# Performance work log

Hardware: AMD Instinct MI355X
Metric: run time of the kernel (lower is better)

Reference implementation:

```python
import jax, jax.numpy as jnp
import numpy as np

B, C, H, W = 1, 256, 96, 96
C8 = C // 8
N = H * W


def setup_inputs() -> dict:
    key = jax.random.key(0)
    ks = jax.random.split(key, 12)
    inp = {
        "x": jax.random.normal(ks[0], (B, C, H, W), jnp.float32),
        "x_encoder": jax.random.normal(ks[1], (B, C, H, W), jnp.float32),
        # 1x1 conv params (weight stored as [out, in] matrices)
        "q_w": jax.random.normal(ks[2], (C8, C), jnp.float32) * 0.05,
        "q_b": jax.random.normal(ks[3], (C8,), jnp.float32) * 0.05,
        "k_w": jax.random.normal(ks[4], (C8, C), jnp.float32) * 0.05,
        "k_b": jax.random.normal(ks[5], (C8,), jnp.float32) * 0.05,
        "v_w": jax.random.normal(ks[6], (C, C), jnp.float32) * 0.05,
        "v_b": jax.random.normal(ks[7], (C,), jnp.float32) * 0.05,
        # positional bias parameters
        "h_pos": jax.random.normal(ks[8], (1, C8, H, 1), jnp.float32),
        "w_pos": jax.random.normal(ks[9], (1, C8, 1, W), jnp.float32),
        # gamma is zero-init in the module; use a random scalar for a non-trivial test
        "gamma": jax.random.normal(ks[10], (1,), jnp.float32),
    }
    return inp


def reference(x, x_encoder, q_w, q_b, k_w, k_b, v_w, v_b, h_pos, w_pos, gamma):
    b, c, h, w = x.shape
    n = h * w
    c8 = q_w.shape[0]
    # 1x1 convs == per-pixel linear maps
    query = (jnp.einsum('bchw,oc->bohw', x, q_w) + q_b[None, :, None, None])
    query = query.reshape(b, c8, n).transpose(0, 2, 1)            # [B, N, C8]
    key = (jnp.einsum('bchw,oc->bohw', x_encoder, k_w) + k_b[None, :, None, None])
    key = key.reshape(b, c8, n)                                   # [B, C8, N]
    # positional bias: broadcast-add then flatten, same as (height+width).view
    pos = (h_pos + w_pos).reshape(1, c8, n)                       # [1, C8, N]
    # energy = Q K^T + Q pos  ==  Q (K + pos)
    energy = jnp.einsum('bnc,bcm->bnm', query, key + pos)         # [B, N, N]
    attention = jax.nn.softmax(energy, axis=-1)
    value = (jnp.einsum('bchw,oc->bohw', x_encoder, v_w) + v_b[None, :, None, None])
    value = value.reshape(b, c, n)                                # [B, C, N]
    out = jnp.einsum('bcm,bnm->bcn', value, attention)            # [B, C, N]
    out = out.reshape(b, c, w, h)  # matches torch .view(B, C, W, H)
    return gamma * out + x
```

## Files before the change

### kernel.cpp

```cpp
#include <hip/hip_runtime.h>
#include <hip/hip_bf16.h>

#define NN 9216
#define CC 256
#define LOG2E 1.4426950408889634f

typedef __attribute__((ext_vector_type(8))) short short8;
typedef __attribute__((ext_vector_type(16))) float floatx16;
typedef __attribute__((ext_vector_type(4))) float floatx4;
typedef __attribute__((ext_vector_type(4))) unsigned short ushortx4;

#if __has_builtin(__builtin_amdgcn_exp2f)
#define fexp2 __builtin_amdgcn_exp2f
#else
#define fexp2 exp2f
#endif

__device__ __forceinline__ unsigned short f2bf(float f) {
    unsigned u = __float_as_uint(f);
    u = u + 0x7fffu + ((u >> 16) & 1u);
    return (unsigned short)(u >> 16);
}
__device__ __forceinline__ float bf2f(unsigned short s) {
    return __uint_as_float(((unsigned)s) << 16);
}
__device__ __forceinline__ unsigned pack2bf(float a, float b) {
    union { __hip_bfloat162 h; unsigned u; } cv;
    cv.h = __float22bfloat162_rn(make_float2(a, b));
    return cv.u;
}
__device__ __forceinline__ floatx16 mfma_bf16(short8 a, short8 b, floatx16 c) {
    return __builtin_amdgcn_mfma_f32_32x32x16_bf16(a, b, c, 0, 0, 0);
}

__global__ __launch_bounds__(256) void prep(
    const float* __restrict__ x, const float* __restrict__ xe,
    short* __restrict__ XBhi, short* __restrict__ XBlo,
    short* __restrict__ EBhi, short* __restrict__ EBlo)
{
    int t = threadIdx.x;
    const float* in = blockIdx.y ? xe : x;
    short* Dhi = blockIdx.y ? EBhi : XBhi;
    short* Dlo = blockIdx.y ? EBlo : XBlo;
    int tl = t & 31, sub = t >> 5;
    int nt = blockIdx.x >> 2, q4 = blockIdx.x & 3;
    int sub2 = q4 * 8 + sub;
    int kb_ = sub2 >> 1, hl = sub2 & 1;
    int n = nt * 32 + tl;
    int c0 = kb_ * 16 + hl * 8;
    union { unsigned short us[8]; short8 v8; } hi, lo;
#pragma unroll
    for (int j = 0; j < 8; ++j) {
        float val = in[(size_t)(c0 + j) * NN + n];
        unsigned short hb = f2bf(val);
        hi.us[j] = hb;
        lo.us[j] = f2bf(val - bf2f(hb));
    }
    size_t off = (((size_t)nt * 16 + kb_) * 64 + hl * 32 + tl) * 8;
    *(short8*)(Dhi + off) = hi.v8;
    *(short8*)(Dlo + off) = lo.v8;
}

__global__ __launch_bounds__(256) void wprep(
    const float* __restrict__ qw, const float* __restrict__ kw,
    const float* __restrict__ vw,
    short* __restrict__ WAhi, short* __restrict__ WAlo)
{
    int g = blockIdx.x * 256 + threadIdx.x;
    int lane = g & 63, kb_ = (g >> 6) & 15, ot = g >> 10;
    int o = lane & 31, half = lane >> 5;
    int c0 = kb_ * 16 + half * 8;
    const float* wsrc;
    int orow;
    float scale = 1.f;
    if (ot == 0) { wsrc = qw; orow = o; scale = LOG2E; }
    else if (ot == 1) { wsrc = kw; orow = o; }
    else { wsrc = vw; orow = (ot - 2) * 32 + o; }
    union { unsigned short us[8]; short8 v8; } hi, lo;
#pragma unroll
    for (int j = 0; j < 8; ++j) {
        float val = wsrc[(size_t)orow * 256 + c0 + j] * scale;
        unsigned short hb = f2bf(val);
        hi.us[j] = hb;
        lo.us[j] = f2bf(val - bf2f(hb));
    }
    size_t off = (((size_t)ot * 16 + kb_) * 64 + lane) * 8;
    *(short8*)(WAhi + off) = hi.v8;
    *(short8*)(WAlo + off) = lo.v8;
}

__global__ __launch_bounds__(256) void gemm_all(
    const short* __restrict__ XBhi, const short* __restrict__ XBlo,
    const short* __restrict__ EBhi, const short* __restrict__ EBlo,
    const short* __restrict__ WAhi, const short* __restrict__ WAlo,
    const float* __restrict__ qb, const float* __restrict__ kb,
    const float* __restrict__ hpos, const float* __restrict__ wpos,
    const float* __restrict__ vb,
    short* __restrict__ Qhi, short* __restrict__ Qlo,
    short* __restrict__ KP2, short* __restrict__ VF)
{
    __shared__ float lds[4][1024];
    int t = threadIdx.x;
    int wv = t >> 6, lane = t & 63, ln = lane & 31, h = lane >> 5;
    int nt = blockIdx.x * 2 + (wv & 1);
    int tile = blockIdx.y * 2 + (wv >> 1);

    const short* Bhi = (tile == 0 ? XBhi : EBhi) + (size_t)nt * 8192 + lane * 8;
    const short* Blo = (tile == 0 ? XBlo : EBlo) + (size_t)nt * 8192 + lane * 8;
    const short* Ahi = WAhi + (size_t)tile * 8192 + lane * 8;
    const short* Alo = WAlo + (size_t)tile * 8192 + lane * 8;

    floatx16 D;
#pragma unroll
    for (int r = 0; r < 16; ++r) D[r] = 0.f;
#pragma unroll
    for (int k = 0; k < 16; ++k) {
        short8 bh = *(const short8*)(Bhi + k * 512);
        short8 bl = *(const short8*)(Blo + k * 512);
        short8 ah = *(const short8*)(Ahi + k * 512);
        short8 al = *(const short8*)(Alo + k * 512);
        D = mfma_bf16(ah, bh, D);
        D = mfma_bf16(ah, bl, D);
        D = mfma_bf16(al, bh, D);
    }

    float* L = lds[wv];
#pragma unroll
    for (int r = 0; r < 16; ++r) {
        int row = (r & 3) + 8 * (r >> 2) + 4 * h;
        L[row * 32 + ((ln + row) & 31)] = D[r];
    }
    __syncthreads();

    if (tile == 0) {
        int n = nt * 32 + ln;
#pragma unroll
        for (int it = 0; it < 2; ++it) {
            int j0 = it * 16 + h * 8;
            union { unsigned short us[8]; short8 v8; } qh_, ql_;
#pragma unroll
            for (int jj = 0; jj < 8; ++jj) {
                int row = j0 + jj;
                float d = L[row * 32 + ((ln + row) & 31)] + qb[row] * LOG2E;
                unsigned short hb = f2bf(d);
                qh_.us[jj] = hb;
                ql_.us[jj] = f2bf(d - bf2f(hb));
            }
            *(short8*)(Qhi + (size_t)n * 32 + j0) = qh_.v8;
            *(short8*)(Qlo + (size_t)n * 32 + j0) = ql_.v8;
        }
    } else if (tile == 1) {
        int n = nt * 32 + ln;
        int hh = ((n >> 5) * 683) >> 11;
        int ww = n - hh * 96;
#pragma unroll
        for (int it = 0; it < 2; ++it) {
            int jb0 = it * 16 + h * 8;
            union { unsigned short us[8]; short8 v8; } o;
#pragma unroll
            for (int jj = 0; jj < 8; ++jj) {
                int row = jb0 + jj;
                float d = L[row * 32 + ((ln + row) & 31)]
                        + kb[row] + hpos[row * 96 + hh] + wpos[row * 96 + ww];
                o.us[jj] = f2bf(d);
            }
            *(short8*)(KP2 + (size_t)nt * 1024 + it * 512 + h * 256 + ln * 8) = o.v8;
        }
    } else {
        int cc = tile - 2;
        float bias = vb[cc * 32 + ln];
#pragma unroll
        for (int it = 0; it < 2; ++it) {
            union { unsigned short us[8]; short8 v8; } o;
#pragma unroll
            for (int ee = 0; ee < 8; ++ee) {
                int ml = it * 16 + h * 8 + ee;
                float d = L[ln * 32 + ((ml + ln) & 31)];
                o.us[ee] = f2bf(d + bias);
            }
            *(short8*)(VF + ((size_t)(nt * 2 + it) * 8 + cc) * 512 + lane * 8) = o.v8;
        }
    }
}

#define FSTEP(AH0, AH1, M0) do {                                                      \
    const size_t mo_ = (size_t)(M0) * 256;                                            \
    short8 va0 = *(const short8*)(Vb + mo_);                                          \
    short8 va1 = *(const short8*)(Vb + mo_ + 512);                                    \
    short8 va2 = *(const short8*)(Vb + mo_ + 1024);                                   \
    short8 va3 = *(const short8*)(Vb + mo_ + 1536);                                   \
    floatx16 S = {0.f,0.f,0.f,0.f,0.f,0.f,0.f,0.f,0.f,0.f,0.f,0.f,0.f,0.f,0.f,0.f};  \
    S = mfma_bf16(AH0, qf00, S);                                                      \
    S = mfma_bf16(AH0, qf01, S);                                                      \
    S = mfma_bf16(AH1, qf10, S);                                                      \
    S = mfma_bf16(AH1, qf11, S);                                                      \
    short8 va4 = *(const short8*)(Vb + mo_ + 2048);                                   \
    short8 va5 = *(const short8*)(Vb + mo_ + 2560);                                   \
    short8 va6 = *(const short8*)(Vb + mo_ + 3072);                                   \
    short8 va7 = *(const short8*)(Vb + mo_ + 3584);                                   \
    float ps = 0.f;                                                                   \
    _Pragma("unroll") for (int r = 0; r < 16; ++r) { S[r] = fexp2(S[r]); ps += S[r]; } \
    ps += __shfl_xor(ps, 32); l_run += ps;                                            \
    unsigned w0 = pack2bf(S[0], S[1]),  w1 = pack2bf(S[2], S[3]);                     \
    unsigned w2 = pack2bf(S[4], S[5]),  w3 = pack2bf(S[6], S[7]);                     \
    unsigned w4 = pack2bf(S[8], S[9]),  w5 = pack2bf(S[10], S[11]);                   \
    unsigned w6 = pack2bf(S[12], S[13]), w7 = pack2bf(S[14], S[15]);                  \
    {   unsigned p0 = h ? w0 : w2, p1 = h ? w1 : w3;                                  \
        unsigned e0 = (unsigned)__shfl_xor((int)p0, 32);                              \
        unsigned e1 = (unsigned)__shfl_xor((int)p1, 32);                              \
        union { unsigned u[4]; short8 v; } pf;                                        \
        pf.u[0] = h ? e0 : w0; pf.u[1] = h ? e1 : w1;                                 \
        pf.u[2] = h ? w2 : e0; pf.u[3] = h ? w3 : e1;                                 \
        O0 = mfma_bf16(va0, pf.v, O0); O1 = mfma_bf16(va1, pf.v, O1);                 \
        O2 = mfma_bf16(va2, pf.v, O2); O3 = mfma_bf16(va3, pf.v, O3);                 \
        O4 = mfma_bf16(va4, pf.v, O4); O5 = mfma_bf16(va5, pf.v, O5);                 \
        O6 = mfma_bf16(va6, pf.v, O6); O7 = mfma_bf16(va7, pf.v, O7); }               \
    short8 vb0 = *(const short8*)(Vb + mo_ + 4096);                                   \
    short8 vb1 = *(const short8*)(Vb + mo_ + 4608);                                   \
    short8 vb2 = *(const short8*)(Vb + mo_ + 5120);                                   \
    short8 vb3 = *(const short8*)(Vb + mo_ + 5632);                                   \
    short8 vb4 = *(const short8*)(Vb + mo_ + 6144);                                   \
    short8 vb5 = *(const short8*)(Vb + mo_ + 6656);                                   \
    short8 vb6 = *(const short8*)(Vb + mo_ + 7168);                                   \
    short8 vb7 = *(const short8*)(Vb + mo_ + 7680);                                   \
    {   unsigned p0 = h ? w4 : w6, p1 = h ? w5 : w7;                                  \
        unsigned e0 = (unsigned)__shfl_xor((int)p0, 32);                              \
        unsigned e1 = (unsigned)__shfl_xor((int)p1, 32);                              \
        union { unsigned u[4]; short8 v; } pf;                                        \
        pf.u[0] = h ? e0 : w4; pf.u[1] = h ? e1 : w5;                                 \
        pf.u[2] = h ? w6 : e0; pf.u[3] = h ? w7 : e1;                                 \
        O0 = mfma_bf16(vb0, pf.v, O0); O1 = mfma_bf16(vb1, pf.v, O1);                 \
        O2 = mfma_bf16(vb2, pf.v, O2); O3 = mfma_bf16(vb3, pf.v, O3);                 \
        O4 = mfma_bf16(vb4, pf.v, O4); O5 = mfma_bf16(vb5, pf.v, O5);                 \
        O6 = mfma_bf16(vb6, pf.v, O6); O7 = mfma_bf16(vb7, pf.v, O7); }               \
} while (0)

#define OGW(G, OG) { _Pragma("unroll") for (int r = 0; r < 16; ++r) { \
    int row = 32*(G) + (r & 3) + 8 * (r >> 2) + 4 * h;                \
    Opart[obase + (size_t)row * NN + n0 + ln] = f2bf(OG[r]); } }

__global__ __launch_bounds__(128, 2) void flash(
    const short* __restrict__ Qhi, const short* __restrict__ Qlo,
    const short* __restrict__ KP2, const short* __restrict__ VT2,
    unsigned short* __restrict__ Opart, float* __restrict__ Lpart,
    int mqmask, int mshift, int mlen)
{
    int t = threadIdx.x;
    int wv = t >> 6;
    int lane = t & 63;
    int ln = lane & 31;
    int h = lane >> 5;
    int nt = blockIdx.x >> mshift, mq = blockIdx.x & mqmask;
    int n0 = nt * 64 + wv * 32;
    int mstart = mq * mlen;

    int qoff = (n0 + ln) * 32 + h * 8;
    short8 qf00 = *(const short8*)(Qhi + qoff);
    short8 qf10 = *(const short8*)(Qhi + qoff + 16);
    short8 qf01 = *(const short8*)(Qlo + qoff);
    short8 qf11 = *(const short8*)(Qlo + qoff + 16);

    const short* Vb  = VT2 + (size_t)mstart * 256 + (size_t)lane * 8;
    const short* KPb = KP2 + (size_t)mstart * 32 + (size_t)lane * 8;

    floatx16 O0, O1, O2, O3, O4, O5, O6, O7;
#pragma unroll
    for (int r = 0; r < 16; ++r) {
        O0[r] = 0.f; O1[r] = 0.f; O2[r] = 0.f; O3[r] = 0.f;
        O4[r] = 0.f; O5[r] = 0.f; O6[r] = 0.f; O7[r] = 0.f;
    }
    float l_run = 0.f;

    short8 ahA0 = *(const short8*)(KPb);
    short8 ahA1 = *(const short8*)(KPb + 512);
    short8 ahB0, ahB1;

    int nsp = mlen >> 6;
    for (int sp = 0; sp < nsp; ++sp) {
        int m0 = sp * 64;
        ahB0 = *(const short8*)(KPb + (size_t)(m0 + 32) * 32);
        ahB1 = *(const short8*)(KPb + (size_t)(m0 + 32) * 32 + 512);
        FSTEP(ahA0, ahA1, m0);
        int nm = (sp < nsp - 1) ? (m0 + 64) : 0;
        ahA0 = *(const short8*)(KPb + (size_t)nm * 32);
        ahA1 = *(const short8*)(KPb + (size_t)nm * 32 + 512);
        FSTEP(ahB0, ahB1, m0 + 32);
    }

    if (lane < 32) Lpart[mq * NN + n0 + ln] = l_run;
    size_t obase = (size_t)mq * ((size_t)CC * NN);
    OGW(0, O0) OGW(1, O1) OGW(2, O2) OGW(3, O3)
    OGW(4, O4) OGW(5, O5) OGW(6, O6) OGW(7, O7)
}

__global__ __launch_bounds__(256) void combine(
    const unsigned short* __restrict__ Opart, const float* __restrict__ Lpart,
    const float* __restrict__ gamma, const float* __restrict__ x,
    float* __restrict__ out, int nparts)
{
    int i = blockIdx.x * 256 + threadIdx.x;
    int flat = i * 4;
    int n = flat % NN;
    floatx4 acc = *(const floatx4*)&x[flat];
    float Ls0 = 0.f, Ls1 = 0.f, Ls2 = 0.f, Ls3 = 0.f;
    float s0 = 0.f, s1 = 0.f, s2 = 0.f, s3 = 0.f;
    for (int q = 0; q < nparts; ++q) {
        floatx4 Lq = *(const floatx4*)&Lpart[q * NN + n];
        Ls0 += Lq[0]; Ls1 += Lq[1]; Ls2 += Lq[2]; Ls3 += Lq[3];
        ushortx4 o = *(const ushortx4*)(Opart + (size_t)q * ((size_t)CC * NN) + flat);
        s0 += bf2f(o[0]); s1 += bf2f(o[1]); s2 += bf2f(o[2]); s3 += bf2f(o[3]);
    }
    float g = gamma[0];
    acc[0] += s0 * (g / Ls0);
    acc[1] += s1 * (g / Ls1);
    acc[2] += s2 * (g / Ls2);
    acc[3] += s3 * (g / Ls3);
    *(floatx4*)&out[flat] = acc;
}

extern "C" void kernel_launch(void* const* d_in, const int* in_sizes, int n_in,
                              void* d_out, int out_size, void* d_ws, size_t ws_size,
                              hipStream_t stream) {
    const float* x  = (const float*)d_in[0];
    const float* xe = (const float*)d_in[1];
    const float* qw = (const float*)d_in[2];
    const float* qb = (const float*)d_in[3];
    const float* kw = (const float*)d_in[4];
    const float* kb = (const float*)d_in[5];
    const float* vw = (const float*)d_in[6];
    const float* vb = (const float*)d_in[7];
    const float* hp = (const float*)d_in[8];
    const float* wp = (const float*)d_in[9];
    const float* gm = (const float*)d_in[10];

    char* ws = (char*)d_ws;
    short* Qhi  = (short*)(ws + 0);
    short* Qlo  = (short*)(ws + 589824);
    short* KP2  = (short*)(ws + 1179648);
    short* WAhi = (short*)(ws + 1769472);
    short* WAlo = (short*)(ws + 1933312);
    short* VF   = (short*)(ws + 2097152);

    const size_t OPART_OFF = 6815744;
    const size_t PART_BYTES = (size_t)CC * NN * 2;
    int nparts = 4, mshift = 2;
    size_t need8 = OPART_OFF + 8 * PART_BYTES + (size_t)8 * NN * 4;
    if (ws_size >= need8) { nparts = 8; mshift = 3; }
    unsigned short* Opart = (unsigned short*)(ws + OPART_OFF);
    float* Lpart = (float*)(ws + OPART_OFF + (size_t)nparts * PART_BYTES);

    short* XBhi = (short*)(ws + OPART_OFF);
    short* XBlo = (short*)(ws + OPART_OFF + 4718592);
    short* EBhi = (short*)(ws + OPART_OFF + 2 * 4718592);
    short* EBlo = (short*)(ws + OPART_OFF + 3 * 4718592);

    prep<<<dim3(1152, 2), dim3(256), 0, stream>>>(x, xe, XBhi, XBlo, EBhi, EBlo);
    wprep<<<dim3(40), dim3(256), 0, stream>>>(qw, kw, vw, WAhi, WAlo);
    gemm_all<<<dim3(144, 5), dim3(256), 0, stream>>>(
        XBhi, XBlo, EBhi, EBlo, WAhi, WAlo, qb, kb, hp, wp, vb, Qhi, Qlo, KP2, VF);
    flash<<<dim3(144 * nparts), dim3(128), 0, stream>>>(
        Qhi, Qlo, KP2, VF, Opart, Lpart, nparts - 1, mshift, NN / nparts);
    combine<<<dim3(2304), dim3(256), 0, stream>>>(Opart, Lpart, gm, x, (float*)d_out, nparts);
}
```

Baseline: 114.1 us.

## Split flash attention into producer/consumer warps sharing probabilities via LDS

The flash kernel moves from 2 waves that each handle 32 queries across all 256 value channels to 4 waves per 64 queries. Each wave computes the exp(QK) scores for one 32-key chunk and writes bf16 probabilities into a double-buffered LDS tile. Every wave then consumes all four chunks for its own 64 channels, so the V fragments each wave loads are reused across 64 queries and accumulator registers drop. In exchange it adds LDS traffic, a barrier every 128 keys, and a cross-wave reduction of the row sums.

```diff
diff --git a/kernel.cpp b/kernel.cpp
--- a/kernel.cpp
+++ b/kernel.cpp
@@ -183,114 +183,136 @@
     }
 }
 
-#define FSTEP(AH0, AH1, M0) do {                                                      \
-    const size_t mo_ = (size_t)(M0) * 256;                                            \
-    short8 va0 = *(const short8*)(Vb + mo_);                                          \
-    short8 va1 = *(const short8*)(Vb + mo_ + 512);                                    \
-    short8 va2 = *(const short8*)(Vb + mo_ + 1024);                                   \
-    short8 va3 = *(const short8*)(Vb + mo_ + 1536);                                   \
-    floatx16 S = {0.f,0.f,0.f,0.f,0.f,0.f,0.f,0.f,0.f,0.f,0.f,0.f,0.f,0.f,0.f,0.f};  \
-    S = mfma_bf16(AH0, qf00, S);                                                      \
-    S = mfma_bf16(AH0, qf01, S);                                                      \
-    S = mfma_bf16(AH1, qf10, S);                                                      \
-    S = mfma_bf16(AH1, qf11, S);                                                      \
-    short8 va4 = *(const short8*)(Vb + mo_ + 2048);                                   \
-    short8 va5 = *(const short8*)(Vb + mo_ + 2560);                                   \
-    short8 va6 = *(const short8*)(Vb + mo_ + 3072);                                   \
-    short8 va7 = *(const short8*)(Vb + mo_ + 3584);                                   \
-    float ps = 0.f;                                                                   \
-    _Pragma("unroll") for (int r = 0; r < 16; ++r) { S[r] = fexp2(S[r]); ps += S[r]; } \
-    ps += __shfl_xor(ps, 32); l_run += ps;                                            \
-    unsigned w0 = pack2bf(S[0], S[1]),  w1 = pack2bf(S[2], S[3]);                     \
-    unsigned w2 = pack2bf(S[4], S[5]),  w3 = pack2bf(S[6], S[7]);                     \
-    unsigned w4 = pack2bf(S[8], S[9]),  w5 = pack2bf(S[10], S[11]);                   \
-    unsigned w6 = pack2bf(S[12], S[13]), w7 = pack2bf(S[14], S[15]);                  \
-    {   unsigned p0 = h ? w0 : w2, p1 = h ? w1 : w3;                                  \
-        unsigned e0 = (unsigned)__shfl_xor((int)p0, 32);                              \
-        unsigned e1 = (unsigned)__shfl_xor((int)p1, 32);                              \
-        union { unsigned u[4]; short8 v; } pf;                                        \
-        pf.u[0] = h ? e0 : w0; pf.u[1] = h ? e1 : w1;                                 \
-        pf.u[2] = h ? w2 : e0; pf.u[3] = h ? w3 : e1;                                 \
-        O0 = mfma_bf16(va0, pf.v, O0); O1 = mfma_bf16(va1, pf.v, O1);                 \
-        O2 = mfma_bf16(va2, pf.v, O2); O3 = mfma_bf16(va3, pf.v, O3);                 \
-        O4 = mfma_bf16(va4, pf.v, O4); O5 = mfma_bf16(va5, pf.v, O5);                 \
-        O6 = mfma_bf16(va6, pf.v, O6); O7 = mfma_bf16(va7, pf.v, O7); }               \
-    short8 vb0 = *(const short8*)(Vb + mo_ + 4096);                                   \
-    short8 vb1 = *(const short8*)(Vb + mo_ + 4608);                                   \
-    short8 vb2 = *(const short8*)(Vb + mo_ + 5120);                                   \
-    short8 vb3 = *(const short8*)(Vb + mo_ + 5632);                                   \
-    short8 vb4 = *(const short8*)(Vb + mo_ + 6144);                                   \
-    short8 vb5 = *(const short8*)(Vb + mo_ + 6656);                                   \
-    short8 vb6 = *(const short8*)(Vb + mo_ + 7168);                                   \
-    short8 vb7 = *(const short8*)(Vb + mo_ + 7680);                                   \
-    {   unsigned p0 = h ? w4 : w6, p1 = h ? w5 : w7;                                  \
-        unsigned e0 = (unsigned)__shfl_xor((int)p0, 32);                              \
-        unsigned e1 = (unsigned)__shfl_xor((int)p1, 32);                              \
-        union { unsigned u[4]; short8 v; } pf;                                        \
-        pf.u[0] = h ? e0 : w4; pf.u[1] = h ? e1 : w5;                                 \
-        pf.u[2] = h ? w6 : e0; pf.u[3] = h ? w7 : e1;                                 \
-        O0 = mfma_bf16(vb0, pf.v, O0); O1 = mfma_bf16(vb1, pf.v, O1);                 \
-        O2 = mfma_bf16(vb2, pf.v, O2); O3 = mfma_bf16(vb3, pf.v, O3);                 \
-        O4 = mfma_bf16(vb4, pf.v, O4); O5 = mfma_bf16(vb5, pf.v, O5);                 \
-        O6 = mfma_bf16(vb6, pf.v, O6); O7 = mfma_bf16(vb7, pf.v, O7); }               \
+#define PRODUCE(CH, BUF) do {                                                      \
+    const short* kp_ = KPb + (size_t)(CH) * 1024;                                  \
+    short8 ah0_ = *(const short8*)(kp_);                                           \
+    short8 ah1_ = *(const short8*)(kp_ + 512);                                     \
+    floatx16 SA = {0.f,0.f,0.f,0.f,0.f,0.f,0.f,0.f,0.f,0.f,0.f,0.f,0.f,0.f,0.f,0.f}; \
+    SA = mfma_bf16(ah0_, qAh0, SA);                                                \
+    SA = mfma_bf16(ah0_, qAl0, SA);                                                \
+    SA = mfma_bf16(ah1_, qAh1, SA);                                                \
+    SA = mfma_bf16(ah1_, qAl1, SA);                                                \
+    floatx16 SB = {0.f,0.f,0.f,0.f,0.f,0.f,0.f,0.f,0.f,0.f,0.f,0.f,0.f,0.f,0.f,0.f}; \
+    SB = mfma_bf16(ah0_, qBh0, SB);                                                \
+    SB = mfma_bf16(ah0_, qBl0, SB);                                                \
+    SB = mfma_bf16(ah1_, qBh1, SB);                                                \
+    SB = mfma_bf16(ah1_, qBl1, SB);                                                \
+    float psA = 0.f, psB = 0.f;                                                    \
+    _Pragma("unroll") for (int r = 0; r < 16; ++r) { SA[r] = fexp2(SA[r]); psA += SA[r]; } \
+    _Pragma("unroll") for (int r = 0; r < 16; ++r) { SB[r] = fexp2(SB[r]); psB += SB[r]; } \
+    psA += __shfl_xor(psA, 32); lA += psA;                                         \
+    psB += __shfl_xor(psB, 32); lB += psB;                                         \
+    char* pb_ = &P_lds[BUF][w][0] + ln * 72 + 8 * h;                               \
+    {   unsigned long long g0 = (unsigned long long)pack2bf(SA[0], SA[1])          \
+                              | ((unsigned long long)pack2bf(SA[2], SA[3]) << 32); \
+        unsigned long long g1 = (unsigned long long)pack2bf(SA[4], SA[5])          \
+                              | ((unsigned long long)pack2bf(SA[6], SA[7]) << 32); \
+        unsigned long long g2 = (unsigned long long)pack2bf(SA[8], SA[9])          \
+                              | ((unsigned long long)pack2bf(SA[10], SA[11]) << 32); \
+        unsigned long long g3 = (unsigned long long)pack2bf(SA[12], SA[13])        \
+                              | ((unsigned long long)pack2bf(SA[14], SA[15]) << 32); \
+        *(unsigned long long*)(pb_)      = g0;                                     \
+        *(unsigned long long*)(pb_ + 16) = g1;                                     \
+        *(unsigned long long*)(pb_ + 32) = g2;                                     \
+        *(unsigned long long*)(pb_ + 48) = g3; }                                   \
+    {   unsigned long long g0 = (unsigned long long)pack2bf(SB[0], SB[1])          \
+                              | ((unsigned long long)pack2bf(SB[2], SB[3]) << 32); \
+        unsigned long long g1 = (unsigned long long)pack2bf(SB[4], SB[5])          \
+                              | ((unsigned long long)pack2bf(SB[6], SB[7]) << 32); \
+        unsigned long long g2 = (unsigned long long)pack2bf(SB[8], SB[9])          \
+                              | ((unsigned long long)pack2bf(SB[10], SB[11]) << 32); \
+        unsigned long long g3 = (unsigned long long)pack2bf(SB[12], SB[13])        \
+                              | ((unsigned long long)pack2bf(SB[14], SB[15]) << 32); \
+        *(unsigned long long*)(pb_ + 2304)      = g0;                              \
+        *(unsigned long long*)(pb_ + 2304 + 16) = g1;                              \
+        *(unsigned long long*)(pb_ + 2304 + 32) = g2;                              \
+        *(unsigned long long*)(pb_ + 2304 + 48) = g3; }                            \
 } while (0)
 
-#define OGW(G, OG) { _Pragma("unroll") for (int r = 0; r < 16; ++r) { \
-    int row = 32*(G) + (r & 3) + 8 * (r >> 2) + 4 * h;                \
-    Opart[obase + (size_t)row * NN + n0 + ln] = f2bf(OG[r]); } }
-
-__global__ __launch_bounds__(128, 2) void flash(
+#define CONSUME(SLOT, BUF, CH) do {                                                \
+    const short* v_ = Vb + (size_t)(CH) * 8192;                                    \
+    short8 v00 = *(const short8*)(v_);                                \
+    short8 v01 = *(const short8*)(v_ + 512);                          \
+    short8 v10 = *(const short8*)(v_ + 4096);                         \
+    short8 v11 = *(const short8*)(v_ + 4096 + 512);                   \
+    const char* pr_ = &P_lds[BUF][SLOT][0] + ln * 72 + h * 16;                     \
+    short8 p0A = *(const short8*)(pr_);                                            \
+    short8 p1A = *(const short8*)(pr_ + 32);                                       \
+    short8 p0B = *(const short8*)(pr_ + 2304);                                     \
+    short8 p1B = *(const short8*)(pr_ + 2304 + 32);                                \
+    OA0 = mfma_bf16(v00, p0A, OA0); OA1 = mfma_bf16(v01, p0A, OA1);                \
+    OB0 = mfma_bf16(v00, p0B, OB0); OB1 = mfma_bf16(v01, p0B, OB1);                \
+    OA0 = mfma_bf16(v10, p1A, OA0); OA1 = mfma_bf16(v11, p1A, OA1);                \
+    OB0 = mfma_bf16(v10, p1B, OB0); OB1 = mfma_bf16(v11, p1B, OB1);                \
+} while (0)
+
+#define OGW2(OG, CT, NS) { _Pragma("unroll") for (int r = 0; r < 16; ++r) {        \
+    int row = w * 64 + (CT) * 32 + (r & 3) + 8 * (r >> 2) + 4 * h;                 \
+    Opart[obase + (size_t)row * NN + n0 + (NS) * 32 + ln] = f2bf(OG[r]); } }
+
+__global__ __launch_bounds__(256, 2) void flash(
     const short* __restrict__ Qhi, const short* __restrict__ Qlo,
-    const short* __restrict__ KP2, const short* __restrict__ VT2,
+    const short* __restrict__ KP2, const short* __restrict__ VF,
     unsigned short* __restrict__ Opart, float* __restrict__ Lpart,
     int mqmask, int mshift, int mlen)
 {
+    __shared__ char P_lds[2][4][4608];
+    __shared__ float Lsh[4][2][32];
+
     int t = threadIdx.x;
-    int wv = t >> 6;
-    int lane = t & 63;
-    int ln = lane & 31;
-    int h = lane >> 5;
+    int w = t >> 6;
+    int lane = t & 63, ln = lane & 31, h = lane >> 5;
     int nt = blockIdx.x >> mshift, mq = blockIdx.x & mqmask;
-    int n0 = nt * 64 + wv * 32;
+    int n0 = nt * 64;
     int mstart = mq * mlen;
-
-    int qoff = (n0 + ln) * 32 + h * 8;
-    short8 qf00 = *(const short8*)(Qhi + qoff);
-    short8 qf10 = *(const short8*)(Qhi + qoff + 16);
-    short8 qf01 = *(const short8*)(Qlo + qoff);
-    short8 qf11 = *(const short8*)(Qlo + qoff + 16);
-
-    const short* Vb  = VT2 + (size_t)mstart * 256 + (size_t)lane * 8;
-    const short* KPb = KP2 + (size_t)mstart * 32 + (size_t)lane * 8;
-
-    floatx16 O0, O1, O2, O3, O4, O5, O6, O7;
-#pragma unroll
-    for (int r = 0; r < 16; ++r) {
-        O0[r] = 0.f; O1[r] = 0.f; O2[r] = 0.f; O3[r] = 0.f;
-        O4[r] = 0.f; O5[r] = 0.f; O6[r] = 0.f; O7[r] = 0.f;
-    }
-    float l_run = 0.f;
-
-    short8 ahA0 = *(const short8*)(KPb);
-    short8 ahA1 = *(const short8*)(KPb + 512);
-    short8 ahB0, ahB1;
-
-    int nsp = mlen >> 6;
-    for (int sp = 0; sp < nsp; ++sp) {
-        int m0 = sp * 64;
-        ahB0 = *(const short8*)(KPb + (size_t)(m0 + 32) * 32);
-        ahB1 = *(const short8*)(KPb + (size_t)(m0 + 32) * 32 + 512);
-        FSTEP(ahA0, ahA1, m0);
-        int nm = (sp < nsp - 1) ? (m0 + 64) : 0;
-        ahA0 = *(const short8*)(KPb + (size_t)nm * 32);
-        ahA1 = *(const short8*)(KPb + (size_t)nm * 32 + 512);
-        FSTEP(ahB0, ahB1, m0 + 32);
-    }
-
-    if (lane < 32) Lpart[mq * NN + n0 + ln] = l_run;
+    int nsup = mlen >> 7;
+
+    int qoffA = (n0 + ln) * 32 + h * 8;
+    int qoffB = qoffA + 1024;
+    short8 qAh0 = *(const short8*)(Qhi + qoffA);
+    short8 qAl0 = *(const short8*)(Qlo + qoffA);
+    short8 qAh1 = *(const short8*)(Qhi + qoffA + 16);
+    short8 qAl1 = *(const short8*)(Qlo + qoffA + 16);
+    short8 qBh0 = *(const short8*)(Qhi + qoffB);
+    short8 qBl0 = *(const short8*)(Qlo + qoffB);
+    short8 qBh1 = *(const short8*)(Qhi + qoffB + 16);
+    short8 qBl1 = *(const short8*)(Qlo + qoffB + 16);
+
+    const short* KPb = KP2 + (size_t)mstart * 32 + lane * 8;
+    const short* Vb = VF + ((size_t)(mstart >> 4) + (size_t)w * 0) * 4096
+                         + (size_t)(mstart >> 4) * 0
+                         ;
+    Vb = VF + (size_t)(mstart >> 4) * 4096 + (size_t)(w * 2) * 512 + (size_t)lane * 8;
+
+    floatx16 OA0, OA1, OB0, OB1;
+#pragma unroll
+    for (int r = 0; r < 16; ++r) { OA0[r] = 0.f; OA1[r] = 0.f; OB0[r] = 0.f; OB1[r] = 0.f; }
+    float lA = 0.f, lB = 0.f;
+
+    PRODUCE(w, 0);
+    __syncthreads();
+
+    for (int sp = 0; sp < nsup; ++sp) {
+        int buf = sp & 1;
+        if (sp < nsup - 1) PRODUCE((sp + 1) * 4 + w, buf ^ 1);
+        int c0_ = sp * 4;
+        CONSUME(0, buf, c0_ + 0);
+        CONSUME(1, buf, c0_ + 1);
+        CONSUME(2, buf, c0_ + 2);
+        CONSUME(3, buf, c0_ + 3);
+        __syncthreads();
+    }
+
+    if (lane < 32) { Lsh[w][0][ln] = lA; Lsh[w][1][ln] = lB; }
+    __syncthreads();
+    if (w == 0 && lane < 32) {
+        Lpart[mq * NN + n0 + ln] =
+            Lsh[0][0][ln] + Lsh[1][0][ln] + Lsh[2][0][ln] + Lsh[3][0][ln];
+        Lpart[mq * NN + n0 + 32 + ln] =
+            Lsh[0][1][ln] + Lsh[1][1][ln] + Lsh[2][1][ln] + Lsh[3][1][ln];
+    }
     size_t obase = (size_t)mq * ((size_t)CC * NN);
-    OGW(0, O0) OGW(1, O1) OGW(2, O2) OGW(3, O3)
-    OGW(4, O4) OGW(5, O5) OGW(6, O6) OGW(7, O7)
+    OGW2(OA0, 0, 0) OGW2(OA1, 1, 0) OGW2(OB0, 0, 1) OGW2(OB1, 1, 1)
 }
 
 __global__ __launch_bounds__(256) void combine(
@@ -358,7 +380,7 @@
     wprep<<<dim3(40), dim3(256), 0, stream>>>(qw, kw, vw, WAhi, WAlo);
     gemm_all<<<dim3(144, 5), dim3(256), 0, stream>>>(
         XBhi, XBlo, EBhi, EBlo, WAhi, WAlo, qb, kb, hp, wp, vb, Qhi, Qlo, KP2, VF);
-    flash<<<dim3(144 * nparts), dim3(128), 0, stream>>>(
+    flash<<<dim3(144 * nparts), dim3(256), 0, stream>>>(
         Qhi, Qlo, KP2, VF, Opart, Lpart, nparts - 1, mshift, NN / nparts);
     combine<<<dim3(2304), dim3(256), 0, stream>>>(Opart, Lpart, gm, x, (float*)d_out, nparts);
 }
```

Result: slower. 139.1 us (+21.9%).
